# Kernel optimization log

Measured on AMD Instinct MI355X. Metric: run time of the kernel, lower is better.

## Reference

```python
import jax, jax.numpy as jnp
import numpy as np

N_NODES = 100000
N_EDGES = 1600000
D_IN = 128
D_OUT = 128


def setup_inputs() -> dict:
    key = jax.random.key(0)
    k1, k2, k3, k4, k5 = jax.random.split(key, 5)
    features = jax.random.normal(k1, (N_NODES, D_IN), dtype=jnp.float32)
    weight = jax.random.normal(k2, (D_IN, D_OUT), dtype=jnp.float32)
    edge_val = jax.random.uniform(k3, (N_EDGES,), dtype=jnp.float32)
    edge_row = jax.random.randint(k4, (N_EDGES,), 0, N_NODES, dtype=jnp.int32)
    edge_col = jax.random.randint(k5, (N_EDGES,), 0, N_NODES, dtype=jnp.int32)
    return {"features": features, "weight": weight, "edge_val": edge_val,
            "edge_row": edge_row, "edge_col": edge_col}


def reference(features, weight, edge_val, edge_row, edge_col):
    # support = features @ W   (dense GEMM; torch.spmm with dense-strided lhs)
    support = features @ weight  # [N, D_OUT]
    # output = pre @ support   (sparse COO adjacency spmm)
    msgs = edge_val[:, None] * support[edge_col]  # [E, D_OUT] gather
    output = jax.ops.segment_sum(msgs, edge_row, num_segments=N_NODES)  # scatter-add
    # act == 'relu'; dropout p=0.0 is identity
    return jax.nn.relu(output)
```

## Files before the change

### kernel.cpp

```cpp
#include <hip/hip_runtime.h>
#include <hip/hip_bf16.h>


#define N_NODES 100000
#define N_EDGES 1600000
#define D 128
#define GEMM_BLOCKS ((N_NODES + 63) / 64)
#define CHUNK_A 8192
#define NBLK_A ((N_EDGES + CHUNK_A - 1) / CHUNK_A)
#define BUCKETS ((N_NODES + 127) / 128)
#define N_SCAN (BUCKETS * NBLK_A)
#define SCAN_BLK ((N_SCAN + 1023) / 1024)
#define BCAP 4608

typedef __attribute__((ext_vector_type(8))) short short8;
typedef __attribute__((ext_vector_type(4))) float floatx4;
typedef int  iv2 __attribute__((ext_vector_type(2)));
typedef int  iv4 __attribute__((ext_vector_type(4)));
typedef float fv4 __attribute__((ext_vector_type(4)));

union U16B { uint4 u4; short8 s8; uint u[4]; ushort us[8]; };

__device__ __forceinline__ ushort f32_to_bf16(float f) {
    uint b = __float_as_uint(f);
    return (ushort)((b + 0x7FFFu + ((b >> 16) & 1u)) >> 16);
}
__device__ __forceinline__ float bf16_to_f32(ushort u) {
    return __uint_as_float((uint)u << 16);
}

__device__ __forceinline__ void gemm_body(const float* __restrict__ feat,
                                          const float* __restrict__ W,
                                          ushort* __restrict__ support,
                                          ushort* __restrict__ Bp , int bid) {
    const int tid = threadIdx.x;
    const int wave = tid >> 6, lane = tid & 63;
    const int row0 = bid * 64 + wave * 16;
    const bool active = (row0 < N_NODES);
    const int m = lane & 15, g = lane >> 4;

    floatx4 acc[8];
    const floatx4 z = {0.f, 0.f, 0.f, 0.f};
    #pragma unroll
    for (int t = 0; t < 8; t++) acc[t] = z;

    const float* arow = feat + (size_t)(row0 + m) * D;
    #pragma unroll
    for (int h = 0; h < 2; h++) {
        if (h) __syncthreads();
        for (int e = tid; e < 64 * D; e += 256) {
            int kk = e >> 7, n = e & 127;
            Bp[(((kk >> 3) * D + n) << 3) | (kk & 7)] = f32_to_bf16(W[(h * 64 + kk) * D + n]);
        }
        __syncthreads();
        if (active) {
            #pragma unroll
            for (int ss = 0; ss < 2; ss++) {
                const int s = h * 2 + ss;
                float4 a0 = *(const float4*)(arow + s * 32 + g * 8);
                float4 a1 = *(const float4*)(arow + s * 32 + g * 8 + 4);
                U16B a;
                a.us[0] = f32_to_bf16(a0.x); a.us[1] = f32_to_bf16(a0.y);
                a.us[2] = f32_to_bf16(a0.z); a.us[3] = f32_to_bf16(a0.w);
                a.us[4] = f32_to_bf16(a1.x); a.us[5] = f32_to_bf16(a1.y);
                a.us[6] = f32_to_bf16(a1.z); a.us[7] = f32_to_bf16(a1.w);
                #pragma unroll
                for (int t = 0; t < 8; t++) {
                    const int chunk = (ss * 4 + g) * D + t * 16 + m;
                    U16B b; b.u4 = *(const uint4*)(Bp + chunk * 8);
                    acc[t] = __builtin_amdgcn_mfma_f32_16x16x32_bf16(a.s8, b.s8, acc[t], 0, 0, 0);
                }
            }
        }
    }
    if (active) {
        #pragma unroll
        for (int t = 0; t < 8; t++) {
            #pragma unroll
            for (int r = 0; r < 4; r++) {
                const int row = row0 + g * 4 + r;
                const int col = t * 16 + m;
                support[(size_t)row * D + col] = f32_to_bf16(acc[t][r]);
            }
        }
    }
}

__global__ __launch_bounds__(256) void gemm_kernel(const float* __restrict__ feat,
                                                   const float* __restrict__ W,
                                                   ushort* __restrict__ support) {
    __shared__ ushort Bp[64 * D];
    gemm_body(feat, W, support, Bp, blockIdx.x);
}

__global__ __launch_bounds__(256) void binhist_kernel(const int* __restrict__ edge_row,
                                                      int* __restrict__ histT,
                                                      uint* __restrict__ st) {
    __shared__ int hist[BUCKETS];
    const int tid = threadIdx.x, blk = blockIdx.x;
    if (blk == 0 && tid < 256) st[tid] = 0;
    for (int i = tid; i < BUCKETS; i += 256) hist[i] = 0;
    __syncthreads();
    const int base = blk * CHUNK_A;
    #pragma unroll
    for (int k = 0; k < CHUNK_A / 256; k++) {
        const int e = base + k * 256 + tid;
        if (e < N_EDGES) atomicAdd(&hist[edge_row[e] >> 7], 1);
    }
    __syncthreads();
    for (int i = tid; i < BUCKETS; i += 256) histT[i * NBLK_A + blk] = hist[i];
}

__global__ __launch_bounds__(1024) void scan_kernel(const int* __restrict__ histT,
                                                    int* __restrict__ baseS,
                                                    int* __restrict__ bucketOff,
                                                    uint* __restrict__ st) {
    __shared__ int wsum[16];
    __shared__ int s_run, s_base;
    const int tid = threadIdx.x, b = blockIdx.x;
    const int gid = b * 1024 + tid;
    const int lane = tid & 63, wave = tid >> 6;

    const int v = (gid < N_SCAN) ? histT[gid] : 0;
    int x = v;
    #pragma unroll
    for (int d = 1; d < 64; d <<= 1) {
        int y = __shfl_up(x, d, 64);
        if (lane >= d) x += y;
    }
    if (lane == 63) wsum[wave] = x;
    __syncthreads();
    if (tid == 0) {
        int run = 0;
        #pragma unroll
        for (int w = 0; w < 16; w++) { int t = wsum[w]; wsum[w] = run; run += t; }
        s_run = run;
        __hip_atomic_store(&st[b], (1u << 30) | (uint)run,
                           __ATOMIC_RELEASE, __HIP_MEMORY_SCOPE_AGENT);
    }
    __syncthreads();
    if (wave == 0) {
        int P = 0;
        int base = b;
        bool done = (b == 0);
        while (!done) {
            const int j = base - 1 - lane;
            uint w;
            if (j >= 0) {
                do {
                    w = __hip_atomic_load(&st[j], __ATOMIC_ACQUIRE, __HIP_MEMORY_SCOPE_AGENT);
                } while ((w >> 30) == 0u);
            } else w = 2u << 30;
            const unsigned long long m2 = __ballot((w >> 30) == 2u);
            int contrib;
            if (m2) {
                const int fl = (int)__ffsll(m2) - 1;
                contrib = (lane <= fl) ? (int)(w & 0x3FFFFFFFu) : 0;
                done = true;
            } else {
                contrib = (int)(w & 0x3FFFFFFFu);
                base -= 64;
            }
            #pragma unroll
            for (int mm = 1; mm < 64; mm <<= 1) contrib += __shfl_xor(contrib, mm, 64);
            P += contrib;
        }
        if (lane == 0) {
            __hip_atomic_store(&st[b], (2u << 30) | (uint)(P + s_run),
                               __ATOMIC_RELEASE, __HIP_MEMORY_SCOPE_AGENT);
            s_base = P;
        }
    }
    __syncthreads();
    if (gid < N_SCAN) {
        const int excl = s_base + wsum[wave] + (x - v);
        baseS[gid] = excl;
        const int bucket = gid / NBLK_A;
        if (gid - bucket * NBLK_A == 0) bucketOff[bucket] = excl;
    }
    if (gid == 0) bucketOff[BUCKETS] = N_EDGES;
}

__global__ __launch_bounds__(256) void binscatter_kernel(const int* __restrict__ edge_row,
                                                         const int* __restrict__ edge_col,
                                                         const float* __restrict__ edge_val,
                                                         const int* __restrict__ baseS,
                                                         iv2* __restrict__ sorted) {
    __shared__ int cur[BUCKETS];
    const int tid = threadIdx.x, blk = blockIdx.x;
    for (int i = tid; i < BUCKETS; i += 256) cur[i] = baseS[i * NBLK_A + blk];
    __syncthreads();
    const int base = blk * CHUNK_A;
    #pragma unroll
    for (int k = 0; k < CHUNK_A / 256; k++) {
        const int e = base + k * 256 + tid;
        if (e < N_EDGES) {
            const int r = edge_row[e];
            const int p = atomicAdd(&cur[r >> 7], 1);
            iv2 pk;
            pk.x = ((r & 127) << 17) | edge_col[e];
            pk.y = __float_as_int(edge_val[e]);
            sorted[p] = pk;
        }
    }
}

__global__ __launch_bounds__(256) void bucket_sort_kernel(const int* __restrict__ bucketOff,
                                                          iv2* __restrict__ sorted,
                                                          int* __restrict__ offsets) {
    __shared__ iv2 ebuf[BCAP];
    __shared__ int cnt[128], cur[128];
    __shared__ int wtot;
    const int tid = threadIdx.x, b = blockIdx.x;
    const int s = bucketOff[b], eEnd = bucketOff[b + 1];
    const int nE = eEnd - s;
    if (tid < 128) cnt[tid] = 0;
    __syncthreads();
    for (int i = tid; i < nE; i += 256) {
        iv2 e = sorted[s + i];
        ebuf[i] = e;
        atomicAdd(&cnt[e.x >> 17], 1);
    }
    __syncthreads();
    const int lane = tid & 63;
    const int myc = (tid < 128) ? cnt[tid] : 0;
    int x = myc;
    #pragma unroll
    for (int d = 1; d < 64; d <<= 1) {
        int y = __shfl_up(x, d, 64);
        if (lane >= d) x += y;
    }
    if (tid == 63) wtot = x;
    __syncthreads();
    const int excl = x + ((tid >= 64 && tid < 128) ? wtot : 0) - myc;
    if (tid < 128) cur[tid] = excl;
    const int row = (b << 7) + tid;
    if (tid < 128 && row < N_NODES) offsets[row] = s + excl;
    if (b == BUCKETS - 1 && tid == 0) offsets[N_NODES] = N_EDGES;
    __syncthreads();
    for (int i = tid; i < nE; i += 256) {
        iv2 e = ebuf[i];
        const int rl = e.x >> 17;
        const int p = atomicAdd(&cur[rl], 1);
        iv2 o; o.x = e.x & 0x1FFFF; o.y = e.y;
        sorted[s + p] = o;
    }
}

__global__ __launch_bounds__(256) void accum_kernel(const ushort* __restrict__ support,
                                                    const int* __restrict__ offsets,
                                                    const iv2* __restrict__ epack,
                                                    float* __restrict__ out) {
    const int tid = threadIdx.x;
    const int row  = (blockIdx.x * 256 + tid) >> 4;
    const int part = tid & 15;
    if (row >= N_NODES) return;

    const int start = offsets[row], end = offsets[row + 1];
    float acc0[8], acc1[8];
    #pragma unroll
    for (int i = 0; i < 8; i++) { acc0[i] = 0.f; acc1[i] = 0.f; }

    int e = start;
    if ((e & 1) && e < end) {
        const iv2 pa = epack[e];
        U16B sa; sa.u4 = *(const uint4*)(support + (size_t)pa.x * D + part * 8);
        const float va = __int_as_float(pa.y);
        #pragma unroll
        for (int i = 0; i < 8; i++) acc0[i] += bf16_to_f32(sa.us[i]) * va;
        ++e;
    }
    for (; e + 3 < end; e += 4) {
        const iv4 qa = ((const iv4*)(epack + e))[0];
        const iv4 qb = ((const iv4*)(epack + e))[1];
        U16B s0; s0.u4 = *(const uint4*)(support + (size_t)qa.x * D + part * 8);
        U16B s1; s1.u4 = *(const uint4*)(support + (size_t)qa.z * D + part * 8);
        U16B s2; s2.u4 = *(const uint4*)(support + (size_t)qb.x * D + part * 8);
        U16B s3; s3.u4 = *(const uint4*)(support + (size_t)qb.z * D + part * 8);
        const float v0 = __int_as_float(qa.y);
        const float v1 = __int_as_float(qa.w);
        const float v2 = __int_as_float(qb.y);
        const float v3 = __int_as_float(qb.w);
        #pragma unroll
        for (int i = 0; i < 8; i++) {
            acc0[i] += bf16_to_f32(s0.us[i]) * v0;
            acc1[i] += bf16_to_f32(s1.us[i]) * v1;
            acc0[i] += bf16_to_f32(s2.us[i]) * v2;
            acc1[i] += bf16_to_f32(s3.us[i]) * v3;
        }
    }
    for (; e < end; ++e) {
        const iv2 pa = epack[e];
        U16B sa; sa.u4 = *(const uint4*)(support + (size_t)pa.x * D + part * 8);
        const float va = __int_as_float(pa.y);
        #pragma unroll
        for (int i = 0; i < 8; i++) acc0[i] += bf16_to_f32(sa.us[i]) * va;
    }

    fv4 lo, hi;
    lo.x = fmaxf(acc0[0] + acc1[0], 0.f); lo.y = fmaxf(acc0[1] + acc1[1], 0.f);
    lo.z = fmaxf(acc0[2] + acc1[2], 0.f); lo.w = fmaxf(acc0[3] + acc1[3], 0.f);
    hi.x = fmaxf(acc0[4] + acc1[4], 0.f); hi.y = fmaxf(acc0[5] + acc1[5], 0.f);
    hi.z = fmaxf(acc0[6] + acc1[6], 0.f); hi.w = fmaxf(acc0[7] + acc1[7], 0.f);
    float* dst = out + (size_t)row * D + part * 8;
    __builtin_nontemporal_store(lo, (fv4*)dst);
    __builtin_nontemporal_store(hi, (fv4*)(dst + 4));
}

__global__ __launch_bounds__(256) void zero_f4_kernel(float4* __restrict__ acc, int n4) {
    int i = blockIdx.x * 256 + threadIdx.x;
    if (i < n4) acc[i] = make_float4(0.f, 0.f, 0.f, 0.f);
}
__global__ __launch_bounds__(256) void spmm_kernel(const ushort* __restrict__ support,
                                                   const float* __restrict__ edge_val,
                                                   const int* __restrict__ edge_row,
                                                   const int* __restrict__ edge_col,
                                                   float* __restrict__ out) {
    const long gtid = (long)blockIdx.x * 256 + threadIdx.x;
    const int edge = (int)(gtid >> 4);
    const int part = (int)(gtid & 15);
    if (edge >= N_EDGES) return;
    const int col = edge_col[edge];
    const int row = edge_row[edge];
    const float v = edge_val[edge];
    U16B s; s.u4 = *(const uint4*)(support + (size_t)col * D + part * 8);
    float* dst = out + (size_t)row * D + part * 8;
    #pragma unroll
    for (int i = 0; i < 8; i++) unsafeAtomicAdd(dst + i, bf16_to_f32(s.us[i]) * v);
}
__global__ __launch_bounds__(256) void relu_kernel(float4* __restrict__ out, int n4) {
    int i = blockIdx.x * 256 + threadIdx.x;
    if (i >= n4) return;
    float4 a = out[i];
    a.x = fmaxf(a.x, 0.f); a.y = fmaxf(a.y, 0.f);
    a.z = fmaxf(a.z, 0.f); a.w = fmaxf(a.w, 0.f);
    out[i] = a;
}

extern "C" void kernel_launch(void* const* d_in, const int* in_sizes, int n_in,
                              void* d_out, int out_size, void* d_ws, size_t ws_size,
                              hipStream_t stream) {
    (void)in_sizes; (void)n_in; (void)out_size;
    const float* feat     = (const float*)d_in[0];
    const float* W        = (const float*)d_in[1];
    const float* edge_val = (const float*)d_in[2];
    const int*   edge_row = (const int*)d_in[3];
    const int*   edge_col = (const int*)d_in[4];
    float* out = (float*)d_out;

    char* ws = (char*)d_ws;
    size_t o = 0;
    ushort* support  = (ushort*)(ws + o); o += (size_t)N_NODES * D * sizeof(ushort);
    int*    offsets  = (int*)(ws + o);    o += ((size_t)(N_NODES + 1) * 4 + 15) & ~15ull;
    int*    histT    = (int*)(ws + o);    o += ((size_t)N_SCAN * 4 + 15) & ~15ull;
    int*    baseS    = (int*)(ws + o);    o += ((size_t)N_SCAN * 4 + 15) & ~15ull;
    int*    bucketOff= (int*)(ws + o);    o += ((size_t)(BUCKETS + 1) * 4 + 15) & ~15ull;
    uint*   st       = (uint*)(ws + o);   o += 256 * 4;
    iv2*    sorted   = (iv2*)(ws + o);    o += (size_t)N_EDGES * 8;
    const size_t needed = o;

    if (ws_size >= needed) {
        gemm_kernel<<<GEMM_BLOCKS, 256, 0, stream>>>(feat, W, support);
        binhist_kernel<<<NBLK_A, 256, 0, stream>>>(edge_row, histT, st);
        scan_kernel<<<SCAN_BLK, 1024, 0, stream>>>(histT, baseS, bucketOff, st);
        binscatter_kernel<<<NBLK_A, 256, 0, stream>>>(edge_row, edge_col, edge_val,
                                                      baseS, sorted);
        bucket_sort_kernel<<<BUCKETS, 256, 0, stream>>>(bucketOff, sorted, offsets);
        accum_kernel<<<(N_NODES * 16 + 255) / 256, 256, 0, stream>>>(support, offsets,
                                                                     sorted, out);
    } else {
        const int n4 = N_NODES * D / 4;
        zero_f4_kernel<<<(n4 + 255) / 256, 256, 0, stream>>>((float4*)out, n4);
        gemm_kernel<<<GEMM_BLOCKS, 256, 0, stream>>>(feat, W, support);
        spmm_kernel<<<(int)(((long)N_EDGES * 16 + 255) / 256), 256, 0, stream>>>(
            support, edge_val, edge_row, edge_col, out);
        relu_kernel<<<(n4 + 255) / 256, 256, 0, stream>>>((float4*)out, n4);
    }
}
```

Measured before the change: 273.5 us.

## Replace two-level bucket sort with global-atomic counting sort into CSR

Replaces the blocked bucket histogram, bucket scatter and per-bucket LDS sort with a direct per-row histogram using global atomics, a single exclusive scan over rows, and a scatter that places each edge with a global atomic cursor. Counter zeroing is folded into the GEMM kernel, and edge arrays are read as 4-wide vectors. The accumulation loop gains an 8-edge unrolled path with nontemporal loads of the packed edges. This removes one kernel and a full extra pass over the edge list, at the cost of heavily contended random global atomics and scattered 8-byte writes. Row order within a row becomes nondeterministic, so float summation order may vary between runs.

```diff
diff --git a/kernel.cpp b/kernel.cpp
--- a/kernel.cpp
+++ b/kernel.cpp
@@ -6,12 +6,9 @@
 #define N_EDGES 1600000
 #define D 128
 #define GEMM_BLOCKS ((N_NODES + 63) / 64)
-#define CHUNK_A 8192
-#define NBLK_A ((N_EDGES + CHUNK_A - 1) / CHUNK_A)
-#define BUCKETS ((N_NODES + 127) / 128)
-#define N_SCAN (BUCKETS * NBLK_A)
-#define SCAN_BLK ((N_SCAN + 1023) / 1024)
-#define BCAP 4608
+#define NE4 (N_EDGES / 4)
+#define EDGE_GRID ((NE4 + 255) / 256)
+#define RSCAN_BLK ((N_NODES + 1023) / 1024)
 
 typedef __attribute__((ext_vector_type(8))) short short8;
 typedef __attribute__((ext_vector_type(4))) float floatx4;
@@ -88,32 +85,33 @@
 
 __global__ __launch_bounds__(256) void gemm_kernel(const float* __restrict__ feat,
                                                    const float* __restrict__ W,
-                                                   ushort* __restrict__ support) {
+                                                   ushort* __restrict__ support,
+                                                   int* __restrict__ cnt,
+                                                   uint* __restrict__ st) {
+    if (cnt) {
+        const int z = blockIdx.x * 256 + threadIdx.x;
+        if (z < N_NODES) cnt[z] = 0;
+        if (z < 256) st[z] = 0u;
+    }
     __shared__ ushort Bp[64 * D];
     gemm_body(feat, W, support, Bp, blockIdx.x);
 }
 
-__global__ __launch_bounds__(256) void binhist_kernel(const int* __restrict__ edge_row,
-                                                      int* __restrict__ histT,
-                                                      uint* __restrict__ st) {
-    __shared__ int hist[BUCKETS];
-    const int tid = threadIdx.x, blk = blockIdx.x;
-    if (blk == 0 && tid < 256) st[tid] = 0;
-    for (int i = tid; i < BUCKETS; i += 256) hist[i] = 0;
-    __syncthreads();
-    const int base = blk * CHUNK_A;
-    #pragma unroll
-    for (int k = 0; k < CHUNK_A / 256; k++) {
-        const int e = base + k * 256 + tid;
-        if (e < N_EDGES) atomicAdd(&hist[edge_row[e] >> 7], 1);
-    }
-    __syncthreads();
-    for (int i = tid; i < BUCKETS; i += 256) histT[i * NBLK_A + blk] = hist[i];
-}
-
-__global__ __launch_bounds__(1024) void scan_kernel(const int* __restrict__ histT,
-                                                    int* __restrict__ baseS,
-                                                    int* __restrict__ bucketOff,
+__global__ __launch_bounds__(256) void hist_kernel(const iv4* __restrict__ edge_row4,
+                                                   int* __restrict__ cnt) {
+    const int i = blockIdx.x * 256 + threadIdx.x;
+    if (i < NE4) {
+        const iv4 r = edge_row4[i];
+        atomicAdd(&cnt[r.x], 1);
+        atomicAdd(&cnt[r.y], 1);
+        atomicAdd(&cnt[r.z], 1);
+        atomicAdd(&cnt[r.w], 1);
+    }
+}
+
+__global__ __launch_bounds__(1024) void scan_kernel(const int* __restrict__ cnt,
+                                                    int* __restrict__ offsets,
+                                                    int* __restrict__ cur,
                                                     uint* __restrict__ st) {
     __shared__ int wsum[16];
     __shared__ int s_run, s_base;
@@ -121,7 +119,7 @@
     const int gid = b * 1024 + tid;
     const int lane = tid & 63, wave = tid >> 6;
 
-    const int v = (gid < N_SCAN) ? histT[gid] : 0;
+    const int v = (gid < N_NODES) ? cnt[gid] : 0;
     int x = v;
     #pragma unroll
     for (int d = 1; d < 64; d <<= 1) {
@@ -172,78 +170,32 @@
         }
     }
     __syncthreads();
-    if (gid < N_SCAN) {
+    if (gid < N_NODES) {
         const int excl = s_base + wsum[wave] + (x - v);
-        baseS[gid] = excl;
-        const int bucket = gid / NBLK_A;
-        if (gid - bucket * NBLK_A == 0) bucketOff[bucket] = excl;
-    }
-    if (gid == 0) bucketOff[BUCKETS] = N_EDGES;
-}
-
-__global__ __launch_bounds__(256) void binscatter_kernel(const int* __restrict__ edge_row,
-                                                         const int* __restrict__ edge_col,
-                                                         const float* __restrict__ edge_val,
-                                                         const int* __restrict__ baseS,
-                                                         iv2* __restrict__ sorted) {
-    __shared__ int cur[BUCKETS];
-    const int tid = threadIdx.x, blk = blockIdx.x;
-    for (int i = tid; i < BUCKETS; i += 256) cur[i] = baseS[i * NBLK_A + blk];
-    __syncthreads();
-    const int base = blk * CHUNK_A;
-    #pragma unroll
-    for (int k = 0; k < CHUNK_A / 256; k++) {
-        const int e = base + k * 256 + tid;
-        if (e < N_EDGES) {
-            const int r = edge_row[e];
-            const int p = atomicAdd(&cur[r >> 7], 1);
-            iv2 pk;
-            pk.x = ((r & 127) << 17) | edge_col[e];
-            pk.y = __float_as_int(edge_val[e]);
-            sorted[p] = pk;
-        }
-    }
-}
-
-__global__ __launch_bounds__(256) void bucket_sort_kernel(const int* __restrict__ bucketOff,
-                                                          iv2* __restrict__ sorted,
-                                                          int* __restrict__ offsets) {
-    __shared__ iv2 ebuf[BCAP];
-    __shared__ int cnt[128], cur[128];
-    __shared__ int wtot;
-    const int tid = threadIdx.x, b = blockIdx.x;
-    const int s = bucketOff[b], eEnd = bucketOff[b + 1];
-    const int nE = eEnd - s;
-    if (tid < 128) cnt[tid] = 0;
-    __syncthreads();
-    for (int i = tid; i < nE; i += 256) {
-        iv2 e = sorted[s + i];
-        ebuf[i] = e;
-        atomicAdd(&cnt[e.x >> 17], 1);
-    }
-    __syncthreads();
-    const int lane = tid & 63;
-    const int myc = (tid < 128) ? cnt[tid] : 0;
-    int x = myc;
-    #pragma unroll
-    for (int d = 1; d < 64; d <<= 1) {
-        int y = __shfl_up(x, d, 64);
-        if (lane >= d) x += y;
-    }
-    if (tid == 63) wtot = x;
-    __syncthreads();
-    const int excl = x + ((tid >= 64 && tid < 128) ? wtot : 0) - myc;
-    if (tid < 128) cur[tid] = excl;
-    const int row = (b << 7) + tid;
-    if (tid < 128 && row < N_NODES) offsets[row] = s + excl;
-    if (b == BUCKETS - 1 && tid == 0) offsets[N_NODES] = N_EDGES;
-    __syncthreads();
-    for (int i = tid; i < nE; i += 256) {
-        iv2 e = ebuf[i];
-        const int rl = e.x >> 17;
-        const int p = atomicAdd(&cur[rl], 1);
-        iv2 o; o.x = e.x & 0x1FFFF; o.y = e.y;
-        sorted[s + p] = o;
+        offsets[gid] = excl;
+        cur[gid] = excl;
+    }
+    if (gid == 0) offsets[N_NODES] = N_EDGES;
+}
+
+__global__ __launch_bounds__(256) void scatter_kernel(const iv4* __restrict__ edge_row4,
+                                                      const iv4* __restrict__ edge_col4,
+                                                      const fv4* __restrict__ edge_val4,
+                                                      int* __restrict__ cur,
+                                                      iv2* __restrict__ sorted) {
+    const int i = blockIdx.x * 256 + threadIdx.x;
+    if (i < NE4) {
+        const iv4 r = edge_row4[i];
+        const iv4 c = edge_col4[i];
+        const fv4 v = edge_val4[i];
+        const int p0 = atomicAdd(&cur[r.x], 1);
+        const int p1 = atomicAdd(&cur[r.y], 1);
+        const int p2 = atomicAdd(&cur[r.z], 1);
+        const int p3 = atomicAdd(&cur[r.w], 1);
+        iv2 e0; e0.x = c.x; e0.y = __float_as_int(v.x); sorted[p0] = e0;
+        iv2 e1; e1.x = c.y; e1.y = __float_as_int(v.y); sorted[p1] = e1;
+        iv2 e2; e2.x = c.z; e2.y = __float_as_int(v.z); sorted[p2] = e2;
+        iv2 e3; e3.x = c.w; e3.y = __float_as_int(v.w); sorted[p3] = e3;
     }
 }
 
@@ -263,16 +215,45 @@
 
     int e = start;
     if ((e & 1) && e < end) {
-        const iv2 pa = epack[e];
+        const iv2 pa = __builtin_nontemporal_load(epack + e);
         U16B sa; sa.u4 = *(const uint4*)(support + (size_t)pa.x * D + part * 8);
         const float va = __int_as_float(pa.y);
         #pragma unroll
         for (int i = 0; i < 8; i++) acc0[i] += bf16_to_f32(sa.us[i]) * va;
         ++e;
     }
+    for (; e + 7 < end; e += 8) {
+        const iv4 qa = __builtin_nontemporal_load((const iv4*)(epack + e));
+        const iv4 qb = __builtin_nontemporal_load((const iv4*)(epack + e) + 1);
+        const iv4 qc = __builtin_nontemporal_load((const iv4*)(epack + e) + 2);
+        const iv4 qd = __builtin_nontemporal_load((const iv4*)(epack + e) + 3);
+        U16B s0; s0.u4 = *(const uint4*)(support + (size_t)qa.x * D + part * 8);
+        U16B s1; s1.u4 = *(const uint4*)(support + (size_t)qa.z * D + part * 8);
+        U16B s2; s2.u4 = *(const uint4*)(support + (size_t)qb.x * D + part * 8);
+        U16B s3; s3.u4 = *(const uint4*)(support + (size_t)qb.z * D + part * 8);
+        U16B s4; s4.u4 = *(const uint4*)(support + (size_t)qc.x * D + part * 8);
+        U16B s5; s5.u4 = *(const uint4*)(support + (size_t)qc.z * D + part * 8);
+        U16B s6; s6.u4 = *(const uint4*)(support + (size_t)qd.x * D + part * 8);
+        U16B s7; s7.u4 = *(const uint4*)(support + (size_t)qd.z * D + part * 8);
+        const float v0 = __int_as_float(qa.y), v1 = __int_as_float(qa.w);
+        const float v2 = __int_as_float(qb.y), v3 = __int_as_float(qb.w);
+        const float v4 = __int_as_float(qc.y), v5 = __int_as_float(qc.w);
+        const float v6 = __int_as_float(qd.y), v7 = __int_as_float(qd.w);
+        #pragma unroll
+        for (int i = 0; i < 8; i++) {
+            acc0[i] += bf16_to_f32(s0.us[i]) * v0;
+            acc1[i] += bf16_to_f32(s1.us[i]) * v1;
+            acc0[i] += bf16_to_f32(s2.us[i]) * v2;
+            acc1[i] += bf16_to_f32(s3.us[i]) * v3;
+            acc0[i] += bf16_to_f32(s4.us[i]) * v4;
+            acc1[i] += bf16_to_f32(s5.us[i]) * v5;
+            acc0[i] += bf16_to_f32(s6.us[i]) * v6;
+            acc1[i] += bf16_to_f32(s7.us[i]) * v7;
+        }
+    }
     for (; e + 3 < end; e += 4) {
-        const iv4 qa = ((const iv4*)(epack + e))[0];
-        const iv4 qb = ((const iv4*)(epack + e))[1];
+        const iv4 qa = __builtin_nontemporal_load((const iv4*)(epack + e));
+        const iv4 qb = __builtin_nontemporal_load((const iv4*)(epack + e) + 1);
         U16B s0; s0.u4 = *(const uint4*)(support + (size_t)qa.x * D + part * 8);
         U16B s1; s1.u4 = *(const uint4*)(support + (size_t)qa.z * D + part * 8);
         U16B s2; s2.u4 = *(const uint4*)(support + (size_t)qb.x * D + part * 8);
@@ -290,7 +271,7 @@
         }
     }
     for (; e < end; ++e) {
-        const iv2 pa = epack[e];
+        const iv2 pa = __builtin_nontemporal_load(epack + e);
         U16B sa; sa.u4 = *(const uint4*)(support + (size_t)pa.x * D + part * 8);
         const float va = __int_as_float(pa.y);
         #pragma unroll
@@ -352,26 +333,25 @@
     size_t o = 0;
     ushort* support  = (ushort*)(ws + o); o += (size_t)N_NODES * D * sizeof(ushort);
     int*    offsets  = (int*)(ws + o);    o += ((size_t)(N_NODES + 1) * 4 + 15) & ~15ull;
-    int*    histT    = (int*)(ws + o);    o += ((size_t)N_SCAN * 4 + 15) & ~15ull;
-    int*    baseS    = (int*)(ws + o);    o += ((size_t)N_SCAN * 4 + 15) & ~15ull;
-    int*    bucketOff= (int*)(ws + o);    o += ((size_t)(BUCKETS + 1) * 4 + 15) & ~15ull;
+    int*    cnt      = (int*)(ws + o);    o += ((size_t)N_NODES * 4 + 15) & ~15ull;
+    int*    cur      = (int*)(ws + o);    o += ((size_t)N_NODES * 4 + 15) & ~15ull;
     uint*   st       = (uint*)(ws + o);   o += 256 * 4;
     iv2*    sorted   = (iv2*)(ws + o);    o += (size_t)N_EDGES * 8;
     const size_t needed = o;
 
     if (ws_size >= needed) {
-        gemm_kernel<<<GEMM_BLOCKS, 256, 0, stream>>>(feat, W, support);
-        binhist_kernel<<<NBLK_A, 256, 0, stream>>>(edge_row, histT, st);
-        scan_kernel<<<SCAN_BLK, 1024, 0, stream>>>(histT, baseS, bucketOff, st);
-        binscatter_kernel<<<NBLK_A, 256, 0, stream>>>(edge_row, edge_col, edge_val,
-                                                      baseS, sorted);
-        bucket_sort_kernel<<<BUCKETS, 256, 0, stream>>>(bucketOff, sorted, offsets);
+        gemm_kernel<<<GEMM_BLOCKS, 256, 0, stream>>>(feat, W, support, cnt, st);
+        hist_kernel<<<EDGE_GRID, 256, 0, stream>>>((const iv4*)edge_row, cnt);
+        scan_kernel<<<RSCAN_BLK, 1024, 0, stream>>>(cnt, offsets, cur, st);
+        scatter_kernel<<<EDGE_GRID, 256, 0, stream>>>((const iv4*)edge_row,
+                                                      (const iv4*)edge_col,
+                                                      (const fv4*)edge_val, cur, sorted);
         accum_kernel<<<(N_NODES * 16 + 255) / 256, 256, 0, stream>>>(support, offsets,
                                                                      sorted, out);
     } else {
         const int n4 = N_NODES * D / 4;
         zero_f4_kernel<<<(n4 + 255) / 256, 256, 0, stream>>>((float4*)out, n4);
-        gemm_kernel<<<GEMM_BLOCKS, 256, 0, stream>>>(feat, W, support);
+        gemm_kernel<<<GEMM_BLOCKS, 256, 0, stream>>>(feat, W, support, nullptr, nullptr);
         spmm_kernel<<<(int)(((long)N_EDGES * 16 + 255) / 256), 256, 0, stream>>>(
             support, edge_val, edge_row, edge_col, out);
         relu_kernel<<<(n4 + 255) / 256, 256, 0, stream>>>((float4*)out, n4);
```

Measured after the change: 373.4 us. 36.5% more time.

## Fuse row histogram into GEMM kernel and unroll SpMM accumulation by eight

Applied to the files above, without the earlier changes.

The bucket histogram over edge_row now runs inside the GEMM kernel's first NBLK_A blocks, which removes one kernel launch and lets histogram work overlap with the GEMM. The accumulate kernel gains an 8-edge unrolled loop so more independent gathers are in flight per thread. Edge-pack reads now use nontemporal loads to avoid polluting cache needed for the support rows. Costs are extra shared memory and registers in the GEMM blocks, and more register pressure in the accumulate kernel, either of which can lower occupancy.

```diff
diff --git a/kernel.cpp b/kernel.cpp
--- a/kernel.cpp
+++ b/kernel.cpp
@@ -88,27 +88,30 @@
 
 __global__ __launch_bounds__(256) void gemm_kernel(const float* __restrict__ feat,
                                                    const float* __restrict__ W,
-                                                   ushort* __restrict__ support) {
+                                                   ushort* __restrict__ support,
+                                                   const int* __restrict__ edge_row,
+                                                   int* __restrict__ histT,
+                                                   uint* __restrict__ st) {
     __shared__ ushort Bp[64 * D];
-    gemm_body(feat, W, support, Bp, blockIdx.x);
-}
-
-__global__ __launch_bounds__(256) void binhist_kernel(const int* __restrict__ edge_row,
-                                                      int* __restrict__ histT,
-                                                      uint* __restrict__ st) {
     __shared__ int hist[BUCKETS];
-    const int tid = threadIdx.x, blk = blockIdx.x;
-    if (blk == 0 && tid < 256) st[tid] = 0;
-    for (int i = tid; i < BUCKETS; i += 256) hist[i] = 0;
-    __syncthreads();
-    const int base = blk * CHUNK_A;
-    #pragma unroll
-    for (int k = 0; k < CHUNK_A / 256; k++) {
-        const int e = base + k * 256 + tid;
-        if (e < N_EDGES) atomicAdd(&hist[edge_row[e] >> 7], 1);
-    }
-    __syncthreads();
-    for (int i = tid; i < BUCKETS; i += 256) histT[i * NBLK_A + blk] = hist[i];
+    const int bid = blockIdx.x, tid = threadIdx.x;
+    const bool doHist = (histT != nullptr) && (bid < NBLK_A);
+    if (doHist) {
+        if (bid == 0 && tid < 256) st[tid] = 0u;
+        for (int i = tid; i < BUCKETS; i += 256) hist[i] = 0;
+    }
+    gemm_body(feat, W, support, Bp, bid);
+    if (doHist) {
+        __syncthreads();
+        const int base = bid * CHUNK_A;
+        #pragma unroll
+        for (int k = 0; k < CHUNK_A / 256; k++) {
+            const int e = base + k * 256 + tid;
+            if (e < N_EDGES) atomicAdd(&hist[edge_row[e] >> 7], 1);
+        }
+        __syncthreads();
+        for (int i = tid; i < BUCKETS; i += 256) histT[i * NBLK_A + bid] = hist[i];
+    }
 }
 
 __global__ __launch_bounds__(1024) void scan_kernel(const int* __restrict__ histT,
@@ -263,16 +266,45 @@
 
     int e = start;
     if ((e & 1) && e < end) {
-        const iv2 pa = epack[e];
+        const iv2 pa = __builtin_nontemporal_load(epack + e);
         U16B sa; sa.u4 = *(const uint4*)(support + (size_t)pa.x * D + part * 8);
         const float va = __int_as_float(pa.y);
         #pragma unroll
         for (int i = 0; i < 8; i++) acc0[i] += bf16_to_f32(sa.us[i]) * va;
         ++e;
     }
+    for (; e + 7 < end; e += 8) {
+        const iv4 qa = __builtin_nontemporal_load((const iv4*)(epack + e));
+        const iv4 qb = __builtin_nontemporal_load((const iv4*)(epack + e) + 1);
+        const iv4 qc = __builtin_nontemporal_load((const iv4*)(epack + e) + 2);
+        const iv4 qd = __builtin_nontemporal_load((const iv4*)(epack + e) + 3);
+        U16B s0; s0.u4 = *(const uint4*)(support + (size_t)qa.x * D + part * 8);
+        U16B s1; s1.u4 = *(const uint4*)(support + (size_t)qa.z * D + part * 8);
+        U16B s2; s2.u4 = *(const uint4*)(support + (size_t)qb.x * D + part * 8);
+        U16B s3; s3.u4 = *(const uint4*)(support + (size_t)qb.z * D + part * 8);
+        U16B s4; s4.u4 = *(const uint4*)(support + (size_t)qc.x * D + part * 8);
+        U16B s5; s5.u4 = *(const uint4*)(support + (size_t)qc.z * D + part * 8);
+        U16B s6; s6.u4 = *(const uint4*)(support + (size_t)qd.x * D + part * 8);
+        U16B s7; s7.u4 = *(const uint4*)(support + (size_t)qd.z * D + part * 8);
+        const float v0 = __int_as_float(qa.y), v1 = __int_as_float(qa.w);
+        const float v2 = __int_as_float(qb.y), v3 = __int_as_float(qb.w);
+        const float v4 = __int_as_float(qc.y), v5 = __int_as_float(qc.w);
+        const float v6 = __int_as_float(qd.y), v7 = __int_as_float(qd.w);
+        #pragma unroll
+        for (int i = 0; i < 8; i++) {
+            acc0[i] += bf16_to_f32(s0.us[i]) * v0;
+            acc1[i] += bf16_to_f32(s1.us[i]) * v1;
+            acc0[i] += bf16_to_f32(s2.us[i]) * v2;
+            acc1[i] += bf16_to_f32(s3.us[i]) * v3;
+            acc0[i] += bf16_to_f32(s4.us[i]) * v4;
+            acc1[i] += bf16_to_f32(s5.us[i]) * v5;
+            acc0[i] += bf16_to_f32(s6.us[i]) * v6;
+            acc1[i] += bf16_to_f32(s7.us[i]) * v7;
+        }
+    }
     for (; e + 3 < end; e += 4) {
-        const iv4 qa = ((const iv4*)(epack + e))[0];
-        const iv4 qb = ((const iv4*)(epack + e))[1];
+        const iv4 qa = __builtin_nontemporal_load((const iv4*)(epack + e));
+        const iv4 qb = __builtin_nontemporal_load((const iv4*)(epack + e) + 1);
         U16B s0; s0.u4 = *(const uint4*)(support + (size_t)qa.x * D + part * 8);
         U16B s1; s1.u4 = *(const uint4*)(support + (size_t)qa.z * D + part * 8);
         U16B s2; s2.u4 = *(const uint4*)(support + (size_t)qb.x * D + part * 8);
@@ -290,7 +322,7 @@
         }
     }
     for (; e < end; ++e) {
-        const iv2 pa = epack[e];
+        const iv2 pa = __builtin_nontemporal_load(epack + e);
         U16B sa; sa.u4 = *(const uint4*)(support + (size_t)pa.x * D + part * 8);
         const float va = __int_as_float(pa.y);
         #pragma unroll
@@ -360,8 +392,7 @@
     const size_t needed = o;
 
     if (ws_size >= needed) {
-        gemm_kernel<<<GEMM_BLOCKS, 256, 0, stream>>>(feat, W, support);
-        binhist_kernel<<<NBLK_A, 256, 0, stream>>>(edge_row, histT, st);
+        gemm_kernel<<<GEMM_BLOCKS, 256, 0, stream>>>(feat, W, support, edge_row, histT, st);
         scan_kernel<<<SCAN_BLK, 1024, 0, stream>>>(histT, baseS, bucketOff, st);
         binscatter_kernel<<<NBLK_A, 256, 0, stream>>>(edge_row, edge_col, edge_val,
                                                       baseS, sorted);
@@ -371,7 +402,7 @@
     } else {
         const int n4 = N_NODES * D / 4;
         zero_f4_kernel<<<(n4 + 255) / 256, 256, 0, stream>>>((float4*)out, n4);
-        gemm_kernel<<<GEMM_BLOCKS, 256, 0, stream>>>(feat, W, support);
+        gemm_kernel<<<GEMM_BLOCKS, 256, 0, stream>>>(feat, W, support, nullptr, nullptr, nullptr);
         spmm_kernel<<<(int)(((long)N_EDGES * 16 + 255) / 256), 256, 0, stream>>>(
             support, edge_val, edge_row, edge_col, out);
         relu_kernel<<<(n4 + 255) / 256, 256, 0, stream>>>((float4*)out, n4);
```

New measurement: 267.9 us. -2.0%, faster.

## Fuse histogram into GEMM and merge bucket sort with row accumulation

Applied to the files above, without the earlier changes.

Folds the edge-row histogram into the GEMM kernel's first blocks, so one launch does both. The per-bucket sort and the SpMM accumulation now run as a single 512-thread kernel. Edges stay in shared memory with an index permutation instead of being written back to global memory and re-read through an offsets array. This removes two launches and a full round trip of the sorted edge array. In exchange, the accumulation now uses only one block per 128 rows (about 782 blocks), so there is less parallelism, and shared-memory use per block goes up.

```diff
diff --git a/kernel.cpp b/kernel.cpp
--- a/kernel.cpp
+++ b/kernel.cpp
@@ -88,27 +88,30 @@
 
 __global__ __launch_bounds__(256) void gemm_kernel(const float* __restrict__ feat,
                                                    const float* __restrict__ W,
-                                                   ushort* __restrict__ support) {
+                                                   ushort* __restrict__ support,
+                                                   const int* __restrict__ edge_row,
+                                                   int* __restrict__ histT,
+                                                   uint* __restrict__ st) {
     __shared__ ushort Bp[64 * D];
-    gemm_body(feat, W, support, Bp, blockIdx.x);
-}
-
-__global__ __launch_bounds__(256) void binhist_kernel(const int* __restrict__ edge_row,
-                                                      int* __restrict__ histT,
-                                                      uint* __restrict__ st) {
     __shared__ int hist[BUCKETS];
-    const int tid = threadIdx.x, blk = blockIdx.x;
-    if (blk == 0 && tid < 256) st[tid] = 0;
-    for (int i = tid; i < BUCKETS; i += 256) hist[i] = 0;
-    __syncthreads();
-    const int base = blk * CHUNK_A;
-    #pragma unroll
-    for (int k = 0; k < CHUNK_A / 256; k++) {
-        const int e = base + k * 256 + tid;
-        if (e < N_EDGES) atomicAdd(&hist[edge_row[e] >> 7], 1);
-    }
-    __syncthreads();
-    for (int i = tid; i < BUCKETS; i += 256) histT[i * NBLK_A + blk] = hist[i];
+    const int bid = blockIdx.x, tid = threadIdx.x;
+    const bool doHist = (histT != nullptr) && (bid < NBLK_A);
+    if (doHist) {
+        if (bid == 0 && tid < 256) st[tid] = 0u;
+        for (int i = tid; i < BUCKETS; i += 256) hist[i] = 0;
+    }
+    gemm_body(feat, W, support, Bp, bid);
+    if (doHist) {
+        __syncthreads();
+        const int base = bid * CHUNK_A;
+        #pragma unroll
+        for (int k = 0; k < CHUNK_A / 256; k++) {
+            const int e = base + k * 256 + tid;
+            if (e < N_EDGES) atomicAdd(&hist[edge_row[e] >> 7], 1);
+        }
+        __syncthreads();
+        for (int i = tid; i < BUCKETS; i += 256) histT[i * NBLK_A + bid] = hist[i];
+    }
 }
 
 __global__ __launch_bounds__(1024) void scan_kernel(const int* __restrict__ histT,
@@ -205,18 +208,21 @@
     }
 }
 
-__global__ __launch_bounds__(256) void bucket_sort_kernel(const int* __restrict__ bucketOff,
-                                                          iv2* __restrict__ sorted,
-                                                          int* __restrict__ offsets) {
+__global__ __launch_bounds__(512) void bucket_accum_kernel(const int* __restrict__ bucketOff,
+                                                           const iv2* __restrict__ sorted,
+                                                           const ushort* __restrict__ support,
+                                                           float* __restrict__ out) {
     __shared__ iv2 ebuf[BCAP];
-    __shared__ int cnt[128], cur[128];
+    __shared__ ushort ord[BCAP];
+    __shared__ int cnt[128], rowStart[128], cur[128];
     __shared__ int wtot;
     const int tid = threadIdx.x, b = blockIdx.x;
     const int s = bucketOff[b], eEnd = bucketOff[b + 1];
     const int nE = eEnd - s;
+
     if (tid < 128) cnt[tid] = 0;
     __syncthreads();
-    for (int i = tid; i < nE; i += 256) {
+    for (int i = tid; i < nE; i += 512) {
         iv2 e = sorted[s + i];
         ebuf[i] = e;
         atomicAdd(&cnt[e.x >> 17], 1);
@@ -232,79 +238,69 @@
     }
     if (tid == 63) wtot = x;
     __syncthreads();
-    const int excl = x + ((tid >= 64 && tid < 128) ? wtot : 0) - myc;
-    if (tid < 128) cur[tid] = excl;
-    const int row = (b << 7) + tid;
-    if (tid < 128 && row < N_NODES) offsets[row] = s + excl;
-    if (b == BUCKETS - 1 && tid == 0) offsets[N_NODES] = N_EDGES;
-    __syncthreads();
-    for (int i = tid; i < nE; i += 256) {
-        iv2 e = ebuf[i];
-        const int rl = e.x >> 17;
+    if (tid < 128) {
+        const int excl = x - myc + ((tid >= 64) ? wtot : 0);
+        rowStart[tid] = excl;
+        cur[tid] = excl;
+    }
+    __syncthreads();
+    for (int i = tid; i < nE; i += 512) {
+        const int rl = ebuf[i].x >> 17;
         const int p = atomicAdd(&cur[rl], 1);
-        iv2 o; o.x = e.x & 0x1FFFF; o.y = e.y;
-        sorted[s + p] = o;
-    }
-}
-
-__global__ __launch_bounds__(256) void accum_kernel(const ushort* __restrict__ support,
-                                                    const int* __restrict__ offsets,
-                                                    const iv2* __restrict__ epack,
-                                                    float* __restrict__ out) {
-    const int tid = threadIdx.x;
-    const int row  = (blockIdx.x * 256 + tid) >> 4;
-    const int part = tid & 15;
-    if (row >= N_NODES) return;
-
-    const int start = offsets[row], end = offsets[row + 1];
-    float acc0[8], acc1[8];
-    #pragma unroll
-    for (int i = 0; i < 8; i++) { acc0[i] = 0.f; acc1[i] = 0.f; }
-
-    int e = start;
-    if ((e & 1) && e < end) {
-        const iv2 pa = epack[e];
-        U16B sa; sa.u4 = *(const uint4*)(support + (size_t)pa.x * D + part * 8);
-        const float va = __int_as_float(pa.y);
+        ord[p] = (ushort)i;
+    }
+    __syncthreads();
+
+    const int g = tid >> 4, part = tid & 15;
+    #pragma unroll
+    for (int t = 0; t < 4; t++) {
+        const int rl = g * 4 + t;
+        const int grow = (b << 7) + rl;
+        if (grow >= N_NODES) break;
+        const int rs = rowStart[rl], re = rs + cnt[rl];
+
+        float acc0[8], acc1[8];
         #pragma unroll
-        for (int i = 0; i < 8; i++) acc0[i] += bf16_to_f32(sa.us[i]) * va;
-        ++e;
-    }
-    for (; e + 3 < end; e += 4) {
-        const iv4 qa = ((const iv4*)(epack + e))[0];
-        const iv4 qb = ((const iv4*)(epack + e))[1];
-        U16B s0; s0.u4 = *(const uint4*)(support + (size_t)qa.x * D + part * 8);
-        U16B s1; s1.u4 = *(const uint4*)(support + (size_t)qa.z * D + part * 8);
-        U16B s2; s2.u4 = *(const uint4*)(support + (size_t)qb.x * D + part * 8);
-        U16B s3; s3.u4 = *(const uint4*)(support + (size_t)qb.z * D + part * 8);
-        const float v0 = __int_as_float(qa.y);
-        const float v1 = __int_as_float(qa.w);
-        const float v2 = __int_as_float(qb.y);
-        const float v3 = __int_as_float(qb.w);
-        #pragma unroll
-        for (int i = 0; i < 8; i++) {
-            acc0[i] += bf16_to_f32(s0.us[i]) * v0;
-            acc1[i] += bf16_to_f32(s1.us[i]) * v1;
-            acc0[i] += bf16_to_f32(s2.us[i]) * v2;
-            acc1[i] += bf16_to_f32(s3.us[i]) * v3;
-        }
-    }
-    for (; e < end; ++e) {
-        const iv2 pa = epack[e];
-        U16B sa; sa.u4 = *(const uint4*)(support + (size_t)pa.x * D + part * 8);
-        const float va = __int_as_float(pa.y);
-        #pragma unroll
-        for (int i = 0; i < 8; i++) acc0[i] += bf16_to_f32(sa.us[i]) * va;
-    }
-
-    fv4 lo, hi;
-    lo.x = fmaxf(acc0[0] + acc1[0], 0.f); lo.y = fmaxf(acc0[1] + acc1[1], 0.f);
-    lo.z = fmaxf(acc0[2] + acc1[2], 0.f); lo.w = fmaxf(acc0[3] + acc1[3], 0.f);
-    hi.x = fmaxf(acc0[4] + acc1[4], 0.f); hi.y = fmaxf(acc0[5] + acc1[5], 0.f);
-    hi.z = fmaxf(acc0[6] + acc1[6], 0.f); hi.w = fmaxf(acc0[7] + acc1[7], 0.f);
-    float* dst = out + (size_t)row * D + part * 8;
-    __builtin_nontemporal_store(lo, (fv4*)dst);
-    __builtin_nontemporal_store(hi, (fv4*)(dst + 4));
+        for (int i = 0; i < 8; i++) { acc0[i] = 0.f; acc1[i] = 0.f; }
+
+        int k = rs;
+        for (; k + 3 < re; k += 4) {
+            const int i0 = ord[k], i1 = ord[k + 1], i2 = ord[k + 2], i3 = ord[k + 3];
+            const iv2 e0 = ebuf[i0], e1 = ebuf[i1], e2 = ebuf[i2], e3 = ebuf[i3];
+            U16B s0; s0.u4 = *(const uint4*)(support + (size_t)(e0.x & 0x1FFFF) * D + part * 8);
+            U16B s1; s1.u4 = *(const uint4*)(support + (size_t)(e1.x & 0x1FFFF) * D + part * 8);
+            U16B s2; s2.u4 = *(const uint4*)(support + (size_t)(e2.x & 0x1FFFF) * D + part * 8);
+            U16B s3; s3.u4 = *(const uint4*)(support + (size_t)(e3.x & 0x1FFFF) * D + part * 8);
+            const float v0 = __int_as_float(e0.y);
+            const float v1 = __int_as_float(e1.y);
+            const float v2 = __int_as_float(e2.y);
+            const float v3 = __int_as_float(e3.y);
+            #pragma unroll
+            for (int i = 0; i < 8; i++) {
+                acc0[i] += bf16_to_f32(s0.us[i]) * v0;
+                acc1[i] += bf16_to_f32(s1.us[i]) * v1;
+                acc0[i] += bf16_to_f32(s2.us[i]) * v2;
+                acc1[i] += bf16_to_f32(s3.us[i]) * v3;
+            }
+        }
+        for (; k < re; ++k) {
+            const int i0 = ord[k];
+            const iv2 e0 = ebuf[i0];
+            U16B s0; s0.u4 = *(const uint4*)(support + (size_t)(e0.x & 0x1FFFF) * D + part * 8);
+            const float v0 = __int_as_float(e0.y);
+            #pragma unroll
+            for (int i = 0; i < 8; i++) acc0[i] += bf16_to_f32(s0.us[i]) * v0;
+        }
+
+        fv4 lo, hi;
+        lo.x = fmaxf(acc0[0] + acc1[0], 0.f); lo.y = fmaxf(acc0[1] + acc1[1], 0.f);
+        lo.z = fmaxf(acc0[2] + acc1[2], 0.f); lo.w = fmaxf(acc0[3] + acc1[3], 0.f);
+        hi.x = fmaxf(acc0[4] + acc1[4], 0.f); hi.y = fmaxf(acc0[5] + acc1[5], 0.f);
+        hi.z = fmaxf(acc0[6] + acc1[6], 0.f); hi.w = fmaxf(acc0[7] + acc1[7], 0.f);
+        float* dst = out + (size_t)grow * D + part * 8;
+        __builtin_nontemporal_store(lo, (fv4*)dst);
+        __builtin_nontemporal_store(hi, (fv4*)(dst + 4));
+    }
 }
 
 __global__ __launch_bounds__(256) void zero_f4_kernel(float4* __restrict__ acc, int n4) {
@@ -351,7 +347,6 @@
     char* ws = (char*)d_ws;
     size_t o = 0;
     ushort* support  = (ushort*)(ws + o); o += (size_t)N_NODES * D * sizeof(ushort);
-    int*    offsets  = (int*)(ws + o);    o += ((size_t)(N_NODES + 1) * 4 + 15) & ~15ull;
     int*    histT    = (int*)(ws + o);    o += ((size_t)N_SCAN * 4 + 15) & ~15ull;
     int*    baseS    = (int*)(ws + o);    o += ((size_t)N_SCAN * 4 + 15) & ~15ull;
     int*    bucketOff= (int*)(ws + o);    o += ((size_t)(BUCKETS + 1) * 4 + 15) & ~15ull;
@@ -360,18 +355,15 @@
     const size_t needed = o;
 
     if (ws_size >= needed) {
-        gemm_kernel<<<GEMM_BLOCKS, 256, 0, stream>>>(feat, W, support);
-        binhist_kernel<<<NBLK_A, 256, 0, stream>>>(edge_row, histT, st);
+        gemm_kernel<<<GEMM_BLOCKS, 256, 0, stream>>>(feat, W, support, edge_row, histT, st);
         scan_kernel<<<SCAN_BLK, 1024, 0, stream>>>(histT, baseS, bucketOff, st);
         binscatter_kernel<<<NBLK_A, 256, 0, stream>>>(edge_row, edge_col, edge_val,
                                                       baseS, sorted);
-        bucket_sort_kernel<<<BUCKETS, 256, 0, stream>>>(bucketOff, sorted, offsets);
-        accum_kernel<<<(N_NODES * 16 + 255) / 256, 256, 0, stream>>>(support, offsets,
-                                                                     sorted, out);
+        bucket_accum_kernel<<<BUCKETS, 512, 0, stream>>>(bucketOff, sorted, support, out);
     } else {
         const int n4 = N_NODES * D / 4;
         zero_f4_kernel<<<(n4 + 255) / 256, 256, 0, stream>>>((float4*)out, n4);
-        gemm_kernel<<<GEMM_BLOCKS, 256, 0, stream>>>(feat, W, support);
+        gemm_kernel<<<GEMM_BLOCKS, 256, 0, stream>>>(feat, W, support, nullptr, nullptr, nullptr);
         spmm_kernel<<<(int)(((long)N_EDGES * 16 + 255) / 256), 256, 0, stream>>>(
             support, edge_val, edge_row, edge_col, out);
         relu_kernel<<<(n4 + 255) / 256, 256, 0, stream>>>((float4*)out, n4);
```

New measurement: 264.2 us. -3.4%, faster.
